# Kernel tuning notes

Hardware: AMD Instinct MI355X
Metric: run time of the kernel (lower is better)

Reference implementation:

```python
import jax, jax.numpy as jnp
import numpy as np

IN_FEATURES = 1024
OUT_FEATURES = 1024
N = 8192

def setup_inputs() -> dict:
    key = jax.random.key(0)
    kx, kw, kb = jax.random.split(key, 3)
    x = jax.random.normal(kx, (N, IN_FEATURES), dtype=jnp.float32)
    # nn.Linear default init: U(-1/sqrt(in), 1/sqrt(in))
    bound = 1.0 / np.sqrt(IN_FEATURES)
    W = jax.random.uniform(kw, (OUT_FEATURES, IN_FEATURES), minval=-bound, maxval=bound, dtype=jnp.float32)
    b = jax.random.uniform(kb, (OUT_FEATURES,), minval=-bound, maxval=bound, dtype=jnp.float32)
    return {"x": x, "W": W, "b": b}

def reference(x, W, b):
    # h: [N, D]
    h = x @ W.T + b
    # scores: [N, N]; tanh applied to raw scores, softmax over dim=1 (rows)
    scores = jnp.tanh(h @ h.T)
    attn = jax.nn.softmax(scores, axis=1)
    out = jnp.tanh(attn @ h)
    return out
```

## Files before the change

kernel.cpp:

```cpp
#include <hip/hip_runtime.h>
#include <hip/hip_bf16.h>
#include <cstdint>
#include <cstddef>

typedef __bf16 bf16_t;
typedef __bf16 bf16x4 __attribute__((ext_vector_type(4)));
typedef __bf16 bf16x8 __attribute__((ext_vector_type(8)));
typedef float f32x4 __attribute__((ext_vector_type(4)));
typedef float f32x16 __attribute__((ext_vector_type(16)));
typedef float f32x2 __attribute__((ext_vector_type(2)));
typedef int i32x4 __attribute__((ext_vector_type(4)));
typedef int i32x8 __attribute__((ext_vector_type(8)));

#define NROWS 8192
#define DFEAT 1024
#define BK 32
#define NBLK 64
#define TILE_B (128 * BK)
#define F8TILE 8192
#define NTRI (NBLK * (NBLK + 1) / 2)

typedef __attribute__((address_space(3))) unsigned int lds_uint;
typedef __attribute__((address_space(1))) const unsigned int glb_uint;

__device__ __forceinline__ float fast_tanh(float x) {
  float e = __expf(2.0f * x);
  return 1.0f - 2.0f * __builtin_amdgcn_rcpf(e + 1.0f);
}

__device__ __forceinline__ unsigned pack_fp8x4(float a, float b, float c, float d) {
  unsigned v = 0;
  v = __builtin_amdgcn_cvt_pk_fp8_f32(a, b, v, false);
  v = __builtin_amdgcn_cvt_pk_fp8_f32(c, d, v, true);
  return v;
}

__global__ __launch_bounds__(256) void cast_kernel(const float* __restrict__ in,
                                                   bf16_t* __restrict__ out, int n4) {
  int i = blockIdx.x * 256 + threadIdx.x;
  if (i < n4) {
    float4 v = *(const float4*)(in + i * 4);
    bf16x4 o = {(bf16_t)v.x, (bf16_t)v.y, (bf16_t)v.z, (bf16_t)v.w};
    *(bf16x4*)(out + i * 4) = o;
  }
}

__device__ __forceinline__ void stage_async(const bf16_t* __restrict__ g, int ld,
                                            int row0, int k0, bf16_t* lds,
                                            int wave, int lane) {
#pragma unroll
  for (int t = 0; t < 2; ++t) {
    const int rb = (t * 4 + wave) * 16;
    const bf16_t* gp = g + (size_t)(row0 + rb + (lane >> 2)) * ld + (k0 + (lane & 3) * 8);
    __builtin_amdgcn_global_load_lds((glb_uint*)gp, (lds_uint*)(lds + rb * BK), 16, 0, 0);
  }
}

__device__ __forceinline__ void stage_f8(const uint8_t* __restrict__ g, int ld,
                                         int row0, int k0, uint8_t* lds,
                                         int wave, int lane) {
#pragma unroll
  for (int t = 0; t < 2; ++t) {
    const int rb = (t * 4 + wave) * 16;
    const uint8_t* gp = g + (size_t)(row0 + rb + (lane >> 2)) * ld + (k0 + (lane & 3) * 16);
    __builtin_amdgcn_global_load_lds((glb_uint*)gp, (lds_uint*)(lds + rb * 64), 16, 0, 0);
  }
}

__global__ __launch_bounds__(256) void gemm1_kernel(const bf16_t* __restrict__ xb,
                                                    const bf16_t* __restrict__ Wb,
                                                    const float* __restrict__ bias,
                                                    bf16_t* __restrict__ hout,
                                                    uint8_t* __restrict__ hT8) {
  __shared__ __align__(16) bf16_t smem[4 * TILE_B];
  const int tid = threadIdx.x;
  const int wave = tid >> 6, lane = tid & 63;
  const int wm = wave >> 1, wn = wave & 1;
  const int l15 = lane & 15, quad = lane >> 4;
  const int m0 = blockIdx.x * 128, n0 = blockIdx.y * 128;
  f32x4 acc[4][4] = {};
  const int NIT = DFEAT / BK;
  stage_async(xb, DFEAT, m0, 0, smem, wave, lane);
  stage_async(Wb, DFEAT, n0, 0, smem + TILE_B, wave, lane);
  __syncthreads();
  for (int it = 0; it < NIT; ++it) {
    bf16_t* lA = smem + (it & 1) * 2 * TILE_B;
    bf16_t* lB = lA + TILE_B;
    if (it + 1 < NIT) {
      bf16_t* nA = smem + ((it + 1) & 1) * 2 * TILE_B;
      stage_async(xb, DFEAT, m0, (it + 1) * BK, nA, wave, lane);
      stage_async(Wb, DFEAT, n0, (it + 1) * BK, nA + TILE_B, wave, lane);
    }
    bf16x8 a[4], b[4];
#pragma unroll
    for (int f = 0; f < 4; ++f) {
      a[f] = *(const bf16x8*)(lA + (wm * 64 + f * 16 + l15) * BK + quad * 8);
      b[f] = *(const bf16x8*)(lB + (wn * 64 + f * 16 + l15) * BK + quad * 8);
    }
#pragma unroll
    for (int i = 0; i < 4; ++i)
#pragma unroll
      for (int j = 0; j < 4; ++j)
        acc[i][j] = __builtin_amdgcn_mfma_f32_16x16x32_bf16(a[i], b[j], acc[i][j], 0, 0, 0);
    __syncthreads();
  }
#pragma unroll
  for (int i = 0; i < 4; ++i) {
    int rbase = m0 + wm * 64 + i * 16 + quad * 4;
#pragma unroll
    for (int j = 0; j < 4; ++j) {
      int col = n0 + wn * 64 + j * 16 + l15;
      float bv = bias[col];
      float hv[4];
#pragma unroll
      for (int r = 0; r < 4; ++r) hv[r] = acc[i][j][r] + bv;
#pragma unroll
      for (int r = 0; r < 4; ++r)
        hout[(size_t)(rbase + r) * DFEAT + col] = (bf16_t)hv[r];
      *(unsigned*)(hT8 + (size_t)col * NROWS + rbase) =
          pack_fp8x4(hv[0], hv[1], hv[2], hv[3]);
    }
  }
}

__global__ __launch_bounds__(256) void scores_sym_kernel(const bf16_t* __restrict__ h,
                                                         uint8_t* __restrict__ P,
                                                         float* __restrict__ lsum) {
  __shared__ __align__(16) char smem[128 * 144];
  bf16_t* lA = (bf16_t*)smem;
  bf16_t* lB = (bf16_t*)(smem + 128 * BK * 2);
  uint8_t (*mir)[144] = (uint8_t(*)[144])smem;

  int t = (blockIdx.x & 7) * (NTRI / 8) + (blockIdx.x >> 3);
  int bm = 0;
  while (t >= NBLK - bm) { t -= NBLK - bm; ++bm; }
  const int bn = bm + t;
  const bool offdiag = (bm != bn);
  const int m0 = bm * 128, n0 = bn * 128;

  const int tid = threadIdx.x;
  const int wave = tid >> 6, lane = tid & 63;
  const int wm = wave >> 1, wn = wave & 1;
  const int l15 = lane & 15, quad = lane >> 4;

  f32x4 acc[4][4] = {};
  for (int k0 = 0; k0 < DFEAT; k0 += BK) {
    __syncthreads();
    stage_async(h, DFEAT, m0, k0, lA, wave, lane);
    stage_async(h, DFEAT, n0, k0, lB, wave, lane);
    __syncthreads();
    bf16x8 a[4], b[4];
#pragma unroll
    for (int f = 0; f < 4; ++f) {
      a[f] = *(const bf16x8*)(lA + (wm * 64 + f * 16 + l15) * BK + quad * 8);
      b[f] = *(const bf16x8*)(lB + (wn * 64 + f * 16 + l15) * BK + quad * 8);
    }
#pragma unroll
    for (int i = 0; i < 4; ++i)
#pragma unroll
      for (int j = 0; j < 4; ++j)
        acc[i][j] = __builtin_amdgcn_mfma_f32_16x16x32_bf16(a[i], b[j], acc[i][j], 0, 0, 0);
  }
  __syncthreads();

  float rs[4][4];
  float cs[4];
#pragma unroll
  for (int i = 0; i < 4; ++i)
#pragma unroll
    for (int r = 0; r < 4; ++r) rs[i][r] = 0.f;
#pragma unroll
  for (int j = 0; j < 4; ++j) cs[j] = 0.f;

#pragma unroll
  for (int i = 0; i < 4; ++i) {
    const int rl_loc = wm * 64 + i * 16 + quad * 4;
    const int rbase = m0 + rl_loc;
#pragma unroll
    for (int j = 0; j < 4; ++j) {
      const int cl_loc = wn * 64 + j * 16 + l15;
      const int col = n0 + cl_loc;
      float p[4];
#pragma unroll
      for (int r = 0; r < 4; ++r) p[r] = __expf(fast_tanh(acc[i][j][r]));
      unsigned packed = pack_fp8x4(p[0], p[1], p[2], p[3]);
      f32x2 d0 = __builtin_amdgcn_cvt_pk_f32_fp8(packed, false);
      f32x2 d1 = __builtin_amdgcn_cvt_pk_f32_fp8(packed, true);
      float q[4] = {d0.x, d0.y, d1.x, d1.y};
#pragma unroll
      for (int r = 0; r < 4; ++r) {
        rs[i][r] += q[r];
        cs[j] += q[r];
        P[(size_t)(rbase + r) * NROWS + col] = (uint8_t)(packed >> (8 * r));
      }
      if (offdiag) *(unsigned*)&mir[cl_loc][rl_loc] = packed;
    }
  }

#pragma unroll
  for (int off = 1; off < 16; off <<= 1)
#pragma unroll
    for (int i = 0; i < 4; ++i)
#pragma unroll
      for (int r = 0; r < 4; ++r) rs[i][r] += __shfl_xor(rs[i][r], off, 64);
  if (l15 == 0) {
#pragma unroll
    for (int i = 0; i < 4; ++i) {
      int rbase = m0 + wm * 64 + i * 16 + quad * 4;
#pragma unroll
      for (int r = 0; r < 4; ++r) atomicAdd(&lsum[rbase + r], rs[i][r]);
    }
  }

  if (offdiag) {
#pragma unroll
    for (int off = 16; off < 64; off <<= 1)
#pragma unroll
      for (int j = 0; j < 4; ++j) cs[j] += __shfl_xor(cs[j], off, 64);
    if (quad == 0) {
#pragma unroll
      for (int j = 0; j < 4; ++j)
        atomicAdd(&lsum[n0 + wn * 64 + j * 16 + l15], cs[j]);
    }
    __syncthreads();
#pragma unroll
    for (int it = 0; it < 4; ++it) {
      int q = tid + it * 256;
      int c = q >> 3, r0 = (q & 7) * 16;
      uint4 v = *(const uint4*)(&mir[c][r0]);
      *(uint4*)(P + (size_t)(n0 + c) * NROWS + m0 + r0) = v;
    }
  }
}

__global__ __launch_bounds__(256) void pv_kernel(const uint8_t* __restrict__ P,
                                                 const uint8_t* __restrict__ hT8,
                                                 const float* __restrict__ lsum,
                                                 float* __restrict__ out) {
  __shared__ __align__(16) uint8_t smem[4 * F8TILE];
  const int tid = threadIdx.x;
  const int wave = tid >> 6, lane = tid & 63;
  const int wm = wave >> 1, wn = wave & 1;
  const int l31 = lane & 31, khalf = lane >> 5;
  const int m0 = blockIdx.x * 128, n0 = blockIdx.y * 128;
  f32x16 acc[2][2] = {};
  const int NIT = NROWS / 64;
  stage_f8(P, NROWS, m0, 0, smem, wave, lane);
  stage_f8(hT8, NROWS, n0, 0, smem + F8TILE, wave, lane);
  __syncthreads();
  for (int it = 0; it < NIT; ++it) {
    uint8_t* lA = smem + (it & 1) * 2 * F8TILE;
    uint8_t* lB = lA + F8TILE;
    if (it + 1 < NIT) {
      uint8_t* nA = smem + ((it + 1) & 1) * 2 * F8TILE;
      stage_f8(P, NROWS, m0, (it + 1) * 64, nA, wave, lane);
      stage_f8(hT8, NROWS, n0, (it + 1) * 64, nA + F8TILE, wave, lane);
    }
    i32x8 a[2], b[2];
#pragma unroll
    for (int f = 0; f < 2; ++f) {
      {
        int off = (wm * 64 + f * 32 + l31) * 64 + khalf * 32;
        i32x4 lo = *(const i32x4*)(lA + off);
        i32x4 hi = *(const i32x4*)(lA + off + 16);
        a[f] = i32x8{lo[0], lo[1], lo[2], lo[3], hi[0], hi[1], hi[2], hi[3]};
      }
      {
        int off = (wn * 64 + f * 32 + l31) * 64 + khalf * 32;
        i32x4 lo = *(const i32x4*)(lB + off);
        i32x4 hi = *(const i32x4*)(lB + off + 16);
        b[f] = i32x8{lo[0], lo[1], lo[2], lo[3], hi[0], hi[1], hi[2], hi[3]};
      }
    }
#pragma unroll
    for (int bi = 0; bi < 2; ++bi)
#pragma unroll
      for (int bj = 0; bj < 2; ++bj)
        acc[bi][bj] = __builtin_amdgcn_mfma_scale_f32_32x32x64_f8f6f4(
            a[bi], b[bj], acc[bi][bj], 0, 0, 0, 0x7F7F7F7F, 0, 0x7F7F7F7F);
    __syncthreads();
  }
#pragma unroll
  for (int bi = 0; bi < 2; ++bi)
#pragma unroll
    for (int bj = 0; bj < 2; ++bj) {
      int cbase = n0 + wn * 64 + bj * 32 + l31;
#pragma unroll
      for (int reg = 0; reg < 16; ++reg) {
        int row = m0 + wm * 64 + bi * 32 + (reg & 3) + 8 * (reg >> 2) + 4 * khalf;
        float rl = __builtin_amdgcn_rcpf(lsum[row]);
        out[(size_t)row * DFEAT + cbase] = fast_tanh(acc[bi][bj][reg] * rl);
      }
    }
}

extern "C" void kernel_launch(void* const* d_in, const int* in_sizes, int n_in,
                              void* d_out, int out_size, void* d_ws, size_t ws_size,
                              hipStream_t stream) {
  const float* x = (const float*)d_in[0];
  const float* W = (const float*)d_in[1];
  const float* bias = (const float*)d_in[2];
  float* out = (float*)d_out;

  bf16_t* xb = (bf16_t*)d_ws;
  bf16_t* Wb = xb + (size_t)NROWS * DFEAT;
  bf16_t* h  = Wb + (size_t)DFEAT * DFEAT;
  uint8_t* hT8 = (uint8_t*)(h + (size_t)NROWS * DFEAT);
  float* lsum = (float*)(hT8 + (size_t)DFEAT * NROWS);
  uint8_t* P = (uint8_t*)(lsum + NROWS);

  cast_kernel<<<(NROWS * DFEAT / 4) / 256, 256, 0, stream>>>(x, xb, NROWS * DFEAT / 4);
  cast_kernel<<<(DFEAT * DFEAT / 4) / 256, 256, 0, stream>>>(W, Wb, DFEAT * DFEAT / 4);
  gemm1_kernel<<<dim3(NROWS / 128, DFEAT / 128), 256, 0, stream>>>(xb, Wb, bias, h, hT8);
  hipMemsetAsync(lsum, 0, NROWS * sizeof(float), stream);
  scores_sym_kernel<<<NTRI, 256, 0, stream>>>(h, P, lsum);
  pv_kernel<<<dim3(NROWS / 128, DFEAT / 128), 256, 0, stream>>>(P, hT8, lsum, out);
}
```

Baseline: 310.9 us.

## Widen symmetric scores tiles to 128x256 with 512-thread blocks

The symmetric scores kernel now covers a 128x256 tile per block with eight waves, launching 1056 blocks instead of 2080 triangular 128x128 tiles. Each A tile loaded into LDS is reused across twice as many columns, which reduces global staging traffic per MFMA. Per-wave flags choose which halves to store and mirror so that diagonal blocks are not double-counted. The cost is more wasted MFMA work on tiles straddling the diagonal, a larger LDS footprint, and a more complex tile-to-block mapping.

```diff
diff --git a/kernel.cpp b/kernel.cpp
--- a/kernel.cpp
+++ b/kernel.cpp
@@ -18,7 +18,7 @@
 #define NBLK 64
 #define TILE_B (128 * BK)
 #define F8TILE 8192
-#define NTRI (NBLK * (NBLK + 1) / 2)
+#define NPAIR 1056
 
 typedef __attribute__((address_space(3))) unsigned int lds_uint;
 typedef __attribute__((address_space(1))) const unsigned int glb_uint;
@@ -123,31 +123,42 @@
   }
 }
 
-__global__ __launch_bounds__(256) void scores_sym_kernel(const bf16_t* __restrict__ h,
+__global__ __launch_bounds__(512) void scores_sym_kernel(const bf16_t* __restrict__ h,
                                                          uint8_t* __restrict__ P,
                                                          float* __restrict__ lsum) {
-  __shared__ __align__(16) char smem[128 * 144];
+  __shared__ __align__(16) char smem[256 * 144];
   bf16_t* lA = (bf16_t*)smem;
-  bf16_t* lB = (bf16_t*)(smem + 128 * BK * 2);
+  bf16_t* lB = (bf16_t*)smem + 128 * BK;
   uint8_t (*mir)[144] = (uint8_t(*)[144])smem;
 
-  int t = (blockIdx.x & 7) * (NTRI / 8) + (blockIdx.x >> 3);
+  int t = (int)(blockIdx.x & 7) * (NPAIR / 8) + (int)(blockIdx.x >> 3);
   int bm = 0;
-  while (t >= NBLK - bm) { t -= NBLK - bm; ++bm; }
-  const int bn = bm + t;
-  const bool offdiag = (bm != bn);
-  const int m0 = bm * 128, n0 = bn * 128;
+  while (t >= 32 - (bm >> 1)) { t -= 32 - (bm >> 1); ++bm; }
+  const int p = (bm >> 1) + t;
+  const int m0 = bm * 128, n0 = p * 256;
+  const bool left_store   = (bm <= 2 * p);
+  const bool left_mirror  = (bm <  2 * p);
+  const bool right_mirror = left_store;
 
   const int tid = threadIdx.x;
   const int wave = tid >> 6, lane = tid & 63;
-  const int wm = wave >> 1, wn = wave & 1;
+  const int wm = wave >> 2, wn = wave & 3;
   const int l15 = lane & 15, quad = lane >> 4;
 
   f32x4 acc[4][4] = {};
   for (int k0 = 0; k0 < DFEAT; k0 += BK) {
     __syncthreads();
-    stage_async(h, DFEAT, m0, k0, lA, wave, lane);
-    stage_async(h, DFEAT, n0, k0, lB, wave, lane);
+    {
+      const int rbA = wave * 16;
+      const bf16_t* gp = h + (size_t)(m0 + rbA + (lane >> 2)) * DFEAT + (k0 + (lane & 3) * 8);
+      __builtin_amdgcn_global_load_lds((glb_uint*)gp, (lds_uint*)(lA + rbA * BK), 16, 0, 0);
+    }
+#pragma unroll
+    for (int t2 = 0; t2 < 2; ++t2) {
+      const int rbB = (t2 * 8 + wave) * 16;
+      const bf16_t* gp = h + (size_t)(n0 + rbB + (lane >> 2)) * DFEAT + (k0 + (lane & 3) * 8);
+      __builtin_amdgcn_global_load_lds((glb_uint*)gp, (lds_uint*)(lB + rbB * BK), 16, 0, 0);
+    }
     __syncthreads();
     bf16x8 a[4], b[4];
 #pragma unroll
@@ -163,6 +174,9 @@
   }
   __syncthreads();
 
+  const bool do_store  = (wn < 2) ? left_store  : true;
+  const bool count_cs  = (wn < 2) ? left_mirror : right_mirror;
+
   float rs[4][4];
   float cs[4];
 #pragma unroll
@@ -180,20 +194,22 @@
     for (int j = 0; j < 4; ++j) {
       const int cl_loc = wn * 64 + j * 16 + l15;
       const int col = n0 + cl_loc;
-      float p[4];
-#pragma unroll
-      for (int r = 0; r < 4; ++r) p[r] = __expf(fast_tanh(acc[i][j][r]));
-      unsigned packed = pack_fp8x4(p[0], p[1], p[2], p[3]);
+      float pp[4];
+#pragma unroll
+      for (int r = 0; r < 4; ++r) pp[r] = __expf(fast_tanh(acc[i][j][r]));
+      unsigned packed = pack_fp8x4(pp[0], pp[1], pp[2], pp[3]);
       f32x2 d0 = __builtin_amdgcn_cvt_pk_f32_fp8(packed, false);
       f32x2 d1 = __builtin_amdgcn_cvt_pk_f32_fp8(packed, true);
       float q[4] = {d0.x, d0.y, d1.x, d1.y};
-#pragma unroll
-      for (int r = 0; r < 4; ++r) {
-        rs[i][r] += q[r];
-        cs[j] += q[r];
-        P[(size_t)(rbase + r) * NROWS + col] = (uint8_t)(packed >> (8 * r));
+      if (do_store) {
+#pragma unroll
+        for (int r = 0; r < 4; ++r) {
+          rs[i][r] += q[r];
+          cs[j] += q[r];
+          P[(size_t)(rbase + r) * NROWS + col] = (uint8_t)(packed >> (8 * r));
+        }
+        if (count_cs) *(unsigned*)&mir[cl_loc][rl_loc] = packed;
       }
-      if (offdiag) *(unsigned*)&mir[cl_loc][rl_loc] = packed;
     }
   }
 
@@ -203,7 +219,7 @@
     for (int i = 0; i < 4; ++i)
 #pragma unroll
       for (int r = 0; r < 4; ++r) rs[i][r] += __shfl_xor(rs[i][r], off, 64);
-  if (l15 == 0) {
+  if (l15 == 0 && do_store) {
 #pragma unroll
     for (int i = 0; i < 4; ++i) {
       int rbase = m0 + wm * 64 + i * 16 + quad * 4;
@@ -212,21 +228,23 @@
     }
   }
 
-  if (offdiag) {
-#pragma unroll
-    for (int off = 16; off < 64; off <<= 1)
-#pragma unroll
-      for (int j = 0; j < 4; ++j) cs[j] += __shfl_xor(cs[j], off, 64);
-    if (quad == 0) {
-#pragma unroll
-      for (int j = 0; j < 4; ++j)
-        atomicAdd(&lsum[n0 + wn * 64 + j * 16 + l15], cs[j]);
-    }
-    __syncthreads();
-#pragma unroll
-    for (int it = 0; it < 4; ++it) {
-      int q = tid + it * 256;
-      int c = q >> 3, r0 = (q & 7) * 16;
+#pragma unroll
+  for (int off = 16; off < 64; off <<= 1)
+#pragma unroll
+    for (int j = 0; j < 4; ++j) cs[j] += __shfl_xor(cs[j], off, 64);
+  if (quad == 0 && count_cs) {
+#pragma unroll
+    for (int j = 0; j < 4; ++j)
+      atomicAdd(&lsum[n0 + wn * 64 + j * 16 + l15], cs[j]);
+  }
+
+  __syncthreads();
+#pragma unroll
+  for (int it2 = 0; it2 < 4; ++it2) {
+    int q2 = tid + it2 * 512;
+    int c = q2 >> 3, r0 = (q2 & 7) * 16;
+    bool dom = (c < 128) ? left_mirror : right_mirror;
+    if (dom) {
       uint4 v = *(const uint4*)(&mir[c][r0]);
       *(uint4*)(P + (size_t)(n0 + c) * NROWS + m0 + r0) = v;
     }
@@ -313,6 +331,6 @@
   cast_kernel<<<(DFEAT * DFEAT / 4) / 256, 256, 0, stream>>>(W, Wb, DFEAT * DFEAT / 4);
   gemm1_kernel<<<dim3(NROWS / 128, DFEAT / 128), 256, 0, stream>>>(xb, Wb, bias, h, hT8);
   hipMemsetAsync(lsum, 0, NROWS * sizeof(float), stream);
-  scores_sym_kernel<<<NTRI, 256, 0, stream>>>(h, P, lsum);
+  scores_sym_kernel<<<NPAIR, 512, 0, stream>>>(h, P, lsum);
   pv_kernel<<<dim3(NROWS / 128, DFEAT / 128), 256, 0, stream>>>(P, hT8, lsum, out);
 }
```

Measured after the change: 324.8 us. 4.5% more time.
